# Kernel optimization log

Hardware: AMD Instinct MI355X
Metric: run time of the kernel (lower is better)

## Reference

```python
import jax, jax.numpy as jnp
import numpy as np

B, N_MAX = 32, 256          # graphs, max nodes per graph (uniform here)
L, D, H, Q, P, F = 4, 256, 8, 4, 16, 32  # layers, hidden, heads, q_dim, pe_dim, phi hidden
NEG = -1e9


def _dense_pos(batch, num_graphs):
    # position of each node inside its (sorted) graph segment
    counts = jax.ops.segment_sum(jnp.ones_like(batch), batch, num_segments=num_graphs)
    starts = jnp.concatenate([jnp.zeros((1,), batch.dtype), jnp.cumsum(counts)[:-1]])
    return jnp.arange(batch.shape[0]) - starts[batch]


def setup_inputs() -> dict:
    key = jax.random.key(0)
    ks = jax.random.split(key, 24)
    N = B * N_MAX
    E = N * 16
    s = 1.0 / np.sqrt(D)
    inp = {
        "x": jax.random.normal(ks[0], (N, D), jnp.float32),
        "z": jax.random.normal(ks[1], (N, Q, P, 2), jnp.float32) * 0.1,
        "Lambda": jax.random.uniform(ks[2], (B, Q, P), jnp.float32),
        "edge_attr": jax.random.normal(ks[3], (E, 16), jnp.float32),
        # attention projections per layer
        "Wq": jax.random.normal(ks[4], (L, D, D), jnp.float32) * s,
        "Wk": jax.random.normal(ks[5], (L, D, D), jnp.float32) * s,
        "Wv": jax.random.normal(ks[6], (L, D, D), jnp.float32) * s,
        "Wo": jax.random.normal(ks[7], (L, D, D), jnp.float32) * s,
        "bq": jnp.zeros((L, D), jnp.float32),
        "bk": jnp.zeros((L, D), jnp.float32),
        "bv": jnp.zeros((L, D), jnp.float32),
        "bo": jnp.zeros((L, D), jnp.float32),
        # eigenvalue MLP (DenseComplexNetwork, SPE-style) per layer
        "phi_W1": jax.random.normal(ks[8], (L, 1, F), jnp.float32),
        "phi_b1": jnp.zeros((L, F), jnp.float32),
        "phi_W2": jax.random.normal(ks[9], (L, F, H), jnp.float32) / np.sqrt(F),
        "phi_b2": jnp.zeros((L, H), jnp.float32),
        # BatchNorm1d affine params per layer
        "bn_gamma": jnp.ones((L, D), jnp.float32),
        "bn_beta": jnp.zeros((L, D), jnp.float32),
        # int inputs
        "edge_index": jax.random.randint(ks[10], (2, E), 0, N),
        "batch": jnp.repeat(jnp.arange(B), N_MAX),
    }
    return inp


def reference(x, z, Lambda, edge_attr, Wq, Wk, Wv, Wo, bq, bk, bv, bo,
              phi_W1, phi_b1, phi_W2, phi_b2, bn_gamma, bn_beta,
              edge_index, batch):
    # edge_index / edge_attr are unused by the original forward as well.
    dh = D // H
    pos = _dense_pos(batch, B)
    mask = jnp.zeros((B, N_MAX), bool).at[batch, pos].set(True)      # [B, n]
    zd = jnp.zeros((B, N_MAX, Q, P, 2), z.dtype).at[batch, pos].set(z)
    zr, zi = zd[..., 0], zd[..., 1]                                   # [B, n, Q, P]

    h0 = x
    for i in range(L):
        # ---- to_dense_batch ----
        hd = jnp.zeros((B, N_MAX, D), x.dtype).at[batch, pos].set(h0)
        # ---- DenseComplexNetwork: phi(Lambda), Re(V diag(phi) V^H) per head ----
        hphi = jax.nn.relu(Lambda[..., None] * phi_W1[i][0] + phi_b1[i])      # [B,Q,P,F]
        phi = jnp.einsum('bqpf,fh->bqph', hphi, phi_W2[i]) + phi_b2[i]        # [B,Q,P,H]
        bias = (jnp.einsum('bqph,biqp,bjqp->bhij', phi, zr, zr)
                + jnp.einsum('bqph,biqp,bjqp->bhij', phi, zi, zi))            # [B,H,n,n]
        # ---- multi-head attention with additive bias + key padding mask ----
        q = (hd @ Wq[i] + bq[i]).reshape(B, N_MAX, H, dh)
        k = (hd @ Wk[i] + bk[i]).reshape(B, N_MAX, H, dh)
        v = (hd @ Wv[i] + bv[i]).reshape(B, N_MAX, H, dh)
        scores = jnp.einsum('bihd,bjhd->bhij', q, k) / jnp.sqrt(jnp.float32(dh)) + bias
        scores = jnp.where(mask[:, None, None, :], scores, NEG)
        attn = jax.nn.softmax(scores, axis=-1)
        o = jnp.einsum('bhij,bjhd->bihd', attn, v).reshape(B, N_MAX, D) @ Wo[i] + bo[i]
        # ---- scatter back (h[mask]), residual, BatchNorm1d (batch stats) ----
        h = o[batch, pos] + h0                                                # [N, D]
        mean = h.mean(axis=0)
        var = ((h - mean) ** 2).mean(axis=0)
        h = (h - mean) / jnp.sqrt(var + 1e-5) * bn_gamma[i] + bn_beta[i]
        h0 = h
    return (h0, z)
```

## Files before the change

### kernel.cpp

```cpp
#include <hip/hip_runtime.h>
#include <hip/hip_bf16.h>

typedef __hip_bfloat16 bf16;
typedef __attribute__((ext_vector_type(8))) short short8v;
typedef __attribute__((ext_vector_type(4))) float f32x4;

constexpr int NB  = 32;
constexpr int NM  = 256;
constexpr int DD  = 256;
constexpr int NH  = 8;
constexpr int QP  = 64;
constexpr int FF  = 32;
constexpr int NT  = NB * NM;
constexpr int HD2 = NT * DD;
constexpr float QSCALE = 0.17677669529663687f;

__device__ __forceinline__ float b2f(unsigned short u) {
  return __uint_as_float(((unsigned)u) << 16);
}
__device__ __forceinline__ short f2b(float f) {
  union { bf16 h; short s; } u;
  u.h = __float2bfloat16(f);
  return u.s;
}

__global__ __launch_bounds__(256) void k_init(const float* __restrict__ z,
                                              float* __restrict__ outz,
                                              short* __restrict__ zbf,
                                              float* __restrict__ bna) {
  const int idx = blockIdx.x * 256 + threadIdx.x;
  const float4 v = ((const float4*)z)[idx];
  ((float4*)outz)[idx] = v;
  short4 s;
  s.x = f2b(v.x); s.y = f2b(v.y); s.z = f2b(v.z); s.w = f2b(v.w);
  ((short4*)zbf)[idx] = s;
  if (idx < 4 * 512) bna[idx] = 0.f;
}

__global__ __launch_bounds__(256) void k_wt(const float* __restrict__ Wq,
                                            const float* __restrict__ Wk,
                                            const float* __restrict__ Wv,
                                            const float* __restrict__ Wo,
                                            short* __restrict__ Wt) {
  __shared__ float Ts[32][33];
  const int mat = blockIdx.x;
  const int l = mat >> 2, wsel = mat & 3;
  const float* W = (wsel == 0 ? Wq : wsel == 1 ? Wk : wsel == 2 ? Wv : Wo) + l * DD * DD;
  const int j0 = blockIdx.y * 32;
  short* out = Wt + (size_t)mat * DD * DD;
  const int t = threadIdx.x;
  const int jj = t & 31, kk8 = t >> 5;
  for (int k0 = 0; k0 < DD; k0 += 32) {
    __syncthreads();
#pragma unroll
    for (int s = 0; s < 4; ++s) {
      const int kl = s * 8 + kk8;
      Ts[kl][jj] = W[(k0 + kl) * DD + j0 + jj];
    }
    __syncthreads();
#pragma unroll
    for (int s = 0; s < 4; ++s) {
      const int jl = (t >> 5) + s * 8;
      const int kl = t & 31;
      out[(size_t)(j0 + jl) * DD + k0 + kl] = f2b(Ts[kl][jl]);
    }
  }
}

__global__ __launch_bounds__(256) void k_phi_all(const float* __restrict__ Lam,
                                                 const float* __restrict__ W1,
                                                 const float* __restrict__ b1,
                                                 const float* __restrict__ W2,
                                                 const float* __restrict__ b2,
                                                 float* __restrict__ phiAll) {
  const int l = blockIdx.y;
  const int t = blockIdx.x * 256 + threadIdx.x;
  const int b = t >> 6, qp = t & 63;
  const float lam = Lam[b * QP + qp];
  const float* w1 = W1 + l * FF;
  const float* bb1 = b1 + l * FF;
  const float* w2 = W2 + l * FF * NH;
  const float* bb2 = b2 + l * NH;
  float acc[NH];
#pragma unroll
  for (int h = 0; h < NH; ++h) acc[h] = bb2[h];
  for (int f = 0; f < FF; ++f) {
    float a = lam * w1[f] + bb1[f];
    a = a > 0.f ? a : 0.f;
#pragma unroll
    for (int h = 0; h < NH; ++h) acc[h] += a * w2[f * NH + h];
  }
#pragma unroll
  for (int h = 0; h < NH; ++h)
    phiAll[(((size_t)l * NB + b) * NH + h) * QP + qp] = acc[h];
}

__global__ __launch_bounds__(256) void k_proj(const float* __restrict__ hsrc,
                                              const short* __restrict__ WtL,
                                              const float* __restrict__ bnstat,
                                              const float* __restrict__ gamma,
                                              const float* __restrict__ beta,
                                              const float* __restrict__ b0,
                                              const float* __restrict__ b1,
                                              const float* __restrict__ b2,
                                              short* __restrict__ o0,
                                              short* __restrict__ o1,
                                              short* __restrict__ o2) {
  __shared__ __align__(16) short As[128 * 128];
  __shared__ __align__(16) short Bs[128 * 128];
  __shared__ float bnsc[256], bnsh[256];
  const int t = threadIdx.x;
  const int m0 = blockIdx.x * 128;
  const int j0 = blockIdx.y * 128;
  const int zz = blockIdx.z;
  const short* W = WtL + (size_t)zz * DD * DD;
  const float* bb = zz == 0 ? b0 : zz == 1 ? b1 : b2;
  short* obf = zz == 0 ? o0 : zz == 1 ? o1 : o2;
  const float scale = (zz == 0) ? QSCALE : 1.0f;

  if (t < 256) {
    float sc = 1.f, sh = 0.f;
    if (bnstat) {
      const float mean = bnstat[t] * (1.0f / NT);
      const float var = bnstat[256 + t] * (1.0f / NT) - mean * mean;
      const float rstd = rsqrtf(var + 1e-5f);
      sc = rstd * gamma[t];
      sh = beta[t] - mean * sc;
    }
    bnsc[t] = sc; bnsh[t] = sh;
  }

  const int lane = t & 63, w = t >> 6;
  const int wr = w >> 1, wc = w & 1;
  const int fr = lane & 15, fq = lane >> 4;

  f32x4 acc[4][4] = {};

  for (int kb = 0; kb < 2; ++kb) {
    __syncthreads();
#pragma unroll
    for (int p = 0; p < 8; ++p) {
      const int c = p * 256 + t;
      const int r = c >> 4, ch = c & 15;
      const int sw = ((ch ^ (r & 7)) << 4);
      const int col0 = kb * 128 + ch * 8;
      const float* src = hsrc + (size_t)(m0 + r) * 256 + col0;
      const float4 v0 = *(const float4*)src;
      const float4 v1 = *(const float4*)(src + 4);
      short8v o;
      o[0] = f2b(v0.x * bnsc[col0 + 0] + bnsh[col0 + 0]);
      o[1] = f2b(v0.y * bnsc[col0 + 1] + bnsh[col0 + 1]);
      o[2] = f2b(v0.z * bnsc[col0 + 2] + bnsh[col0 + 2]);
      o[3] = f2b(v0.w * bnsc[col0 + 3] + bnsh[col0 + 3]);
      o[4] = f2b(v1.x * bnsc[col0 + 4] + bnsh[col0 + 4]);
      o[5] = f2b(v1.y * bnsc[col0 + 5] + bnsh[col0 + 5]);
      o[6] = f2b(v1.z * bnsc[col0 + 6] + bnsh[col0 + 6]);
      o[7] = f2b(v1.w * bnsc[col0 + 7] + bnsh[col0 + 7]);
      *(short8v*)((char*)As + r * 256 + sw) = o;
      *(short8v*)((char*)Bs + r * 256 + sw) =
          *(const short8v*)(W + (size_t)(j0 + r) * 256 + kb * 128 + ch * 8);
    }
    __syncthreads();
#pragma unroll
    for (int ks = 0; ks < 4; ++ks) {
      short8v a[4], bfrag[4];
#pragma unroll
      for (int m = 0; m < 4; ++m) {
        const int rA = wr * 64 + m * 16 + fr;
        a[m] = *(const short8v*)((const char*)As + rA * 256 + (((ks * 4 + fq) ^ (rA & 7)) << 4));
        const int rB = wc * 64 + m * 16 + fr;
        bfrag[m] = *(const short8v*)((const char*)Bs + rB * 256 + (((ks * 4 + fq) ^ (rB & 7)) << 4));
      }
#pragma unroll
      for (int m = 0; m < 4; ++m)
#pragma unroll
        for (int n = 0; n < 4; ++n)
          acc[m][n] = __builtin_amdgcn_mfma_f32_16x16x32_bf16(a[m], bfrag[n], acc[m][n], 0, 0, 0);
    }
  }
#pragma unroll
  for (int n = 0; n < 4; ++n) {
    const int col = j0 + wc * 64 + n * 16 + fr;
    const float bv = bb[col];
#pragma unroll
    for (int m = 0; m < 4; ++m) {
#pragma unroll
      for (int rr = 0; rr < 4; ++rr) {
        const int row = m0 + wr * 64 + m * 16 + fq * 4 + rr;
        obf[(size_t)row * 256 + col] = f2b((acc[m][n][rr] + bv) * scale);
      }
    }
  }
}

__global__ __launch_bounds__(256) void k_projo(const short* __restrict__ Abf,
                                               const short* __restrict__ WtO,
                                               const float* __restrict__ bo,
                                               const float* __restrict__ hin,
                                               float* __restrict__ hout,
                                               const float* __restrict__ bnstat,
                                               const float* __restrict__ gamma,
                                               const float* __restrict__ beta,
                                               float* __restrict__ bna) {
  __shared__ __align__(16) short As[64 * 128];
  __shared__ __align__(16) short Bs[128 * 128];
  __shared__ float sred[2][128][2];
  __shared__ float bnsc[256], bnsh[256];
  const int t = threadIdx.x;
  const int m0 = blockIdx.x * 64;
  const int c0 = blockIdx.y * 128;
  const int lane = t & 63, w = t >> 6;
  const int wr = w >> 1, wc = w & 1;
  const int fr = lane & 15, fq = lane >> 4;

  if (t < 256) {
    float sc = 1.f, sh = 0.f;
    if (bnstat) {
      const float mean = bnstat[t] * (1.0f / NT);
      const float var = bnstat[256 + t] * (1.0f / NT) - mean * mean;
      const float rstd = rsqrtf(var + 1e-5f);
      sc = rstd * gamma[t];
      sh = beta[t] - mean * sc;
    }
    bnsc[t] = sc; bnsh[t] = sh;
  }

  f32x4 acc[2][4] = {};
  for (int kb = 0; kb < 2; ++kb) {
    __syncthreads();
#pragma unroll
    for (int p = 0; p < 4; ++p) {
      const int c = p * 256 + t;
      const int r = c >> 4, ch = c & 15;
      const int sw = ((ch ^ (r & 7)) << 4);
      *(short8v*)((char*)As + r * 256 + sw) =
          *(const short8v*)(Abf + (size_t)(m0 + r) * 256 + kb * 128 + ch * 8);
    }
#pragma unroll
    for (int p = 0; p < 8; ++p) {
      const int c = p * 256 + t;
      const int r = c >> 4, ch = c & 15;
      const int sw = ((ch ^ (r & 7)) << 4);
      *(short8v*)((char*)Bs + r * 256 + sw) =
          *(const short8v*)(WtO + (size_t)(c0 + r) * 256 + kb * 128 + ch * 8);
    }
    __syncthreads();
#pragma unroll
    for (int ks = 0; ks < 4; ++ks) {
      short8v a[2], bfrag[4];
#pragma unroll
      for (int m = 0; m < 2; ++m) {
        const int rA = wr * 32 + m * 16 + fr;
        a[m] = *(const short8v*)((const char*)As + rA * 256 + (((ks * 4 + fq) ^ (rA & 7)) << 4));
      }
#pragma unroll
      for (int n = 0; n < 4; ++n) {
        const int rB = wc * 64 + n * 16 + fr;
        bfrag[n] = *(const short8v*)((const char*)Bs + rB * 256 + (((ks * 4 + fq) ^ (rB & 7)) << 4));
      }
#pragma unroll
      for (int m = 0; m < 2; ++m)
#pragma unroll
        for (int n = 0; n < 4; ++n)
          acc[m][n] = __builtin_amdgcn_mfma_f32_16x16x32_bf16(a[m], bfrag[n], acc[m][n], 0, 0, 0);
    }
  }
#pragma unroll
  for (int n = 0; n < 4; ++n) {
    const int col = c0 + wc * 64 + n * 16 + fr;
    const float bv = bo[col];
    const float sc = bnsc[col], sh = bnsh[col];
    float s = 0.f, ss = 0.f;
#pragma unroll
    for (int m = 0; m < 2; ++m) {
#pragma unroll
      for (int rr = 0; rr < 4; ++rr) {
        const int row = m0 + wr * 32 + m * 16 + fq * 4 + rr;
        const size_t idx = (size_t)row * 256 + col;
        const float v = acc[m][n][rr] + bv + (hin[idx] * sc + sh);
        hout[idx] = v;
        s += v;
        ss += v * v;
      }
    }
    s += __shfl_xor(s, 16); s += __shfl_xor(s, 32);
    ss += __shfl_xor(ss, 16); ss += __shfl_xor(ss, 32);
    if (fq == 0) {
      sred[wr][wc * 64 + n * 16 + fr][0] = s;
      sred[wr][wc * 64 + n * 16 + fr][1] = ss;
    }
  }
  __syncthreads();
  if (t < 128) {
    const float s = sred[0][t][0] + sred[1][t][0];
    const float ss = sred[0][t][1] + sred[1][t][1];
    atomicAdd(&bna[c0 + t], s);
    atomicAdd(&bna[256 + c0 + t], ss);
  }
}

__global__ __launch_bounds__(512, 2) void k_attn2(const short* __restrict__ qbf,
                                                  const short* __restrict__ kbf,
                                                  const short* __restrict__ vbf,
                                                  const short* __restrict__ zbf,
                                                  const float* __restrict__ phiAll,
                                                  short* __restrict__ obf, int l) {
  __shared__ __align__(16) char Ks[256 * 384];
  __shared__ __align__(16) char Vt[32 * 512];
  __shared__ __align__(16) char Pw[8 * 2 * 2560];
  __shared__ float rs_l[8 * 32];
  __shared__ float ph2[128];
  const int t = threadIdx.x;
  const int bh = blockIdx.x;
  const int b = bh >> 3, hh = bh & 7;
  const int bnode = b * 256;

  if (t < 128)
    ph2[t] = phiAll[(((size_t)l * NB + b) * NH + hh) * QP + (t >> 1)];
  __syncthreads();
  {
    const int r = t >> 1, half = t & 1;
    const size_t rowbase = (size_t)(bnode + r) * 256 + hh * 32;
#pragma unroll
    for (int j2 = 0; j2 < 2; ++j2) {
      const int c = half * 2 + j2;
      short8v v = *(const short8v*)(kbf + rowbase + c * 8);
      *(short8v*)(Ks + r * 384 + ((c ^ (r & 7)) << 4)) = v;
    }
    const short* zrow = zbf + (size_t)(bnode + r) * 128 + half * 64;
#pragma unroll
    for (int cc = 0; cc < 8; ++cc) {
      const short8v zv = *(const short8v*)(zrow + cc * 8);
      const int zc = half * 64 + cc * 8;
      short8v o;
#pragma unroll
      for (int e = 0; e < 8; ++e)
        o[e] = f2b(b2f((unsigned short)zv[e]) * ph2[zc + e]);
      const int c = 4 + half * 8 + cc;
      *(short8v*)(Ks + r * 384 + ((c ^ (r & 7)) << 4)) = o;
    }
    const short* vrow = vbf + rowbase + half * 16;
    short8v v0 = *(const short8v*)(vrow);
    short8v v1 = *(const short8v*)(vrow + 8);
#pragma unroll
    for (int dd = 0; dd < 16; ++dd) {
      const int d = half * 16 + dd;
      const short val = dd < 8 ? v0[dd] : v1[dd - 8];
      *(short*)(Vt + d * 512 + (((r >> 3) ^ (d & 7)) << 4) + (r & 7) * 2) = val;
    }
  }
  __syncthreads();

  const int lane = t & 63, w = t >> 6;
  const int fr = lane & 15, fq = lane >> 4;
  const int i0w = w * 32;

  short8v Qf[2][5];
#pragma unroll
  for (int s = 0; s < 2; ++s) {
    const int node = bnode + i0w + s * 16 + fr;
    Qf[s][0] = *(const short8v*)(qbf + (size_t)node * 256 + hh * 32 + fq * 8);
    const short* zr = zbf + (size_t)node * 128;
#pragma unroll
    for (int ks = 1; ks < 5; ++ks)
      Qf[s][ks] = *(const short8v*)(zr + (ks - 1) * 32 + fq * 8);
  }

  f32x4 acc[2][16] = {};
#pragma unroll
  for (int ks = 0; ks < 5; ++ks) {
#pragma unroll
    for (int jt = 0; jt < 16; ++jt) {
      const int row = jt * 16 + fr;
      const short8v a = *(const short8v*)(Ks + row * 384 + (((ks * 4 + fq) ^ (row & 7)) << 4));
      acc[0][jt] = __builtin_amdgcn_mfma_f32_16x16x32_bf16(a, Qf[0][ks], acc[0][jt], 0, 0, 0);
      acc[1][jt] = __builtin_amdgcn_mfma_f32_16x16x32_bf16(a, Qf[1][ks], acc[1][jt], 0, 0, 0);
    }
  }

  float rsv0, rsv1;
#pragma unroll
  for (int s = 0; s < 2; ++s) {
    float m = -1e30f;
#pragma unroll
    for (int jt = 0; jt < 16; ++jt)
#pragma unroll
      for (int rr = 0; rr < 4; ++rr) m = fmaxf(m, acc[s][jt][rr]);
    m = fmaxf(m, __shfl_xor(m, 16));
    m = fmaxf(m, __shfl_xor(m, 32));
    float sm = 0.f;
#pragma unroll
    for (int jt = 0; jt < 16; ++jt)
#pragma unroll
      for (int rr = 0; rr < 4; ++rr) {
        const float e = __expf(acc[s][jt][rr] - m);
        acc[s][jt][rr] = e;
        sm += e;
      }
    sm += __shfl_xor(sm, 16);
    sm += __shfl_xor(sm, 32);
    const float r = 1.0f / sm;
    if (s == 0) rsv0 = r; else rsv1 = r;
  }
  if (fq == 0) rs_l[w * 32 + fr] = rsv0;
  if (fq == 1) rs_l[w * 32 + 16 + fr] = rsv1;

  f32x4 oac[2][2] = {};
  char* pw0 = Pw + w * 5120;
#pragma unroll
  for (int ks = 0; ks < 8; ++ks) {
    char* pw = pw0 + (ks & 1) * 2560;
#pragma unroll
    for (int s = 0; s < 2; ++s) {
#pragma unroll
      for (int j2 = 0; j2 < 2; ++j2) {
        const int jt = ks * 2 + j2;
        short4 pk;
        pk.x = f2b(acc[s][jt][0]); pk.y = f2b(acc[s][jt][1]);
        pk.z = f2b(acc[s][jt][2]); pk.w = f2b(acc[s][jt][3]);
        *(short4*)(pw + (s * 16 + fr) * 80 + j2 * 32 + fq * 8) = pk;
      }
    }
    asm volatile("s_waitcnt lgkmcnt(0)" ::: "memory");
    __builtin_amdgcn_sched_barrier(0);
    const short8v pa0 = *(const short8v*)(pw + fr * 80 + fq * 16);
    const short8v pa1 = *(const short8v*)(pw + (16 + fr) * 80 + fq * 16);
    const int sw = (((ks * 4 + fq) ^ (fr & 7)) << 4);
    const short8v vb0 = *(const short8v*)(Vt + fr * 512 + sw);
    const short8v vb1 = *(const short8v*)(Vt + (16 + fr) * 512 + sw);
    oac[0][0] = __builtin_amdgcn_mfma_f32_16x16x32_bf16(pa0, vb0, oac[0][0], 0, 0, 0);
    oac[0][1] = __builtin_amdgcn_mfma_f32_16x16x32_bf16(pa0, vb1, oac[0][1], 0, 0, 0);
    oac[1][0] = __builtin_amdgcn_mfma_f32_16x16x32_bf16(pa1, vb0, oac[1][0], 0, 0, 0);
    oac[1][1] = __builtin_amdgcn_mfma_f32_16x16x32_bf16(pa1, vb1, oac[1][1], 0, 0, 0);
  }

#pragma unroll
  for (int s = 0; s < 2; ++s) {
#pragma unroll
    for (int rr = 0; rr < 4; ++rr) {
      const float rs = rs_l[w * 32 + s * 16 + fq * 4 + rr];
      const int node = bnode + i0w + s * 16 + fq * 4 + rr;
#pragma unroll
      for (int nt = 0; nt < 2; ++nt)
        obf[(size_t)node * 256 + hh * 32 + nt * 16 + fr] = f2b(oac[s][nt][rr] * rs);
    }
  }
}

__global__ __launch_bounds__(256) void k_bn_apply(const float* __restrict__ h,
                                                  const float* __restrict__ accum,
                                                  const float* __restrict__ gamma,
                                                  const float* __restrict__ beta,
                                                  float* __restrict__ outp, int l) {
  const int idx = blockIdx.x * 256 + threadIdx.x;
  const int col = idx & 255;
  const float mean = accum[col] * (1.0f / NT);
  const float var = accum[DD + col] * (1.0f / NT) - mean * mean;
  const float rstd = rsqrtf(var + 1e-5f);
  outp[idx] = (h[idx] - mean) * rstd * gamma[l * DD + col] + beta[l * DD + col];
}

extern "C" void kernel_launch(void* const* d_in, const int* in_sizes, int n_in,
                              void* d_out, int out_size, void* d_ws, size_t ws_size,
                              hipStream_t stream) {
  (void)in_sizes; (void)n_in; (void)out_size; (void)ws_size;
  const float* x    = (const float*)d_in[0];
  const float* z    = (const float*)d_in[1];
  const float* Lam  = (const float*)d_in[2];
  const float* Wq   = (const float*)d_in[4];
  const float* Wk   = (const float*)d_in[5];
  const float* Wv   = (const float*)d_in[6];
  const float* Wo   = (const float*)d_in[7];
  const float* bq   = (const float*)d_in[8];
  const float* bk   = (const float*)d_in[9];
  const float* bv   = (const float*)d_in[10];
  const float* bo   = (const float*)d_in[11];
  const float* pW1  = (const float*)d_in[12];
  const float* pb1  = (const float*)d_in[13];
  const float* pW2  = (const float*)d_in[14];
  const float* pb2  = (const float*)d_in[15];
  const float* gam  = (const float*)d_in[16];
  const float* bet  = (const float*)d_in[17];
  float* out = (float*)d_out;

  float* h    = (float*)d_ws;
  short* qbf  = (short*)(h + HD2);
  short* kbf  = qbf + HD2;
  short* vbf  = kbf + HD2;
  short* obf  = vbf + HD2;
  short* zbf  = obf + HD2;
  short* Wt   = zbf + NT * 128;
  float* phiA = (float*)(Wt + 16 * DD * DD);
  float* bna  = phiA + 4 * NB * NH * QP;

  k_init<<<1024, 256, 0, stream>>>(z, out + HD2, zbf, bna);
  k_wt<<<dim3(16, 8), 256, 0, stream>>>(Wq, Wk, Wv, Wo, Wt);
  k_phi_all<<<dim3(8, 4), 256, 0, stream>>>(Lam, pW1, pb1, pW2, pb2, phiA);
  for (int l = 0; l < 4; ++l) {
    const float* bnprev = l ? bna + (l - 1) * 512 : nullptr;
    const float* gprev  = l ? gam + (l - 1) * DD : gam;
    const float* bprev  = l ? bet + (l - 1) * DD : bet;
    const float* hsrc   = l ? h : x;
    k_proj<<<dim3(64, 2, 3), 256, 0, stream>>>(hsrc, Wt + (size_t)l * 4 * DD * DD,
                                               bnprev, gprev, bprev,
                                               bq + l * DD, bk + l * DD, bv + l * DD,
                                               qbf, kbf, vbf);
    k_attn2<<<256, 512, 0, stream>>>(qbf, kbf, vbf, zbf, phiA, obf, l);
    k_projo<<<dim3(128, 2), 256, 0, stream>>>(obf, Wt + (size_t)(l * 4 + 3) * DD * DD,
                                              bo + l * DD, hsrc, h,
                                              bnprev, gprev, bprev, bna + l * 512);
  }
  k_bn_apply<<<8192, 256, 0, stream>>>(h, bna + 3 * 512, gam, bet, out, 3);
}
```

Before: 169.4 us.

## Fuse setup kernels and share BN-converted activation tile across QKV projections

Merges the three setup kernels (z copy and bf16 convert, weight transpose, phi MLP) into one launch to cut launch overhead. Replaces the QKV projection kernel, which re-read and re-normalized the fp32 activations once per matrix, with one that loads a 64-row, full-K activation tile once into LDS and loops over Q, K and V weights. This cuts global activation reads and BN/convert work by about a factor of three, but each block now runs three serial GEMMs with smaller M tiles, giving fewer MFMAs per weight load. The grid drops from 384 to 256 blocks.

```diff
diff --git a/kernel.cpp b/kernel.cpp
--- a/kernel.cpp
+++ b/kernel.cpp
@@ -24,100 +24,9 @@
   return u.s;
 }
 
-__global__ __launch_bounds__(256) void k_init(const float* __restrict__ z,
-                                              float* __restrict__ outz,
-                                              short* __restrict__ zbf,
-                                              float* __restrict__ bna) {
-  const int idx = blockIdx.x * 256 + threadIdx.x;
-  const float4 v = ((const float4*)z)[idx];
-  ((float4*)outz)[idx] = v;
-  short4 s;
-  s.x = f2b(v.x); s.y = f2b(v.y); s.z = f2b(v.z); s.w = f2b(v.w);
-  ((short4*)zbf)[idx] = s;
-  if (idx < 4 * 512) bna[idx] = 0.f;
-}
-
-__global__ __launch_bounds__(256) void k_wt(const float* __restrict__ Wq,
-                                            const float* __restrict__ Wk,
-                                            const float* __restrict__ Wv,
-                                            const float* __restrict__ Wo,
-                                            short* __restrict__ Wt) {
-  __shared__ float Ts[32][33];
-  const int mat = blockIdx.x;
-  const int l = mat >> 2, wsel = mat & 3;
-  const float* W = (wsel == 0 ? Wq : wsel == 1 ? Wk : wsel == 2 ? Wv : Wo) + l * DD * DD;
-  const int j0 = blockIdx.y * 32;
-  short* out = Wt + (size_t)mat * DD * DD;
-  const int t = threadIdx.x;
-  const int jj = t & 31, kk8 = t >> 5;
-  for (int k0 = 0; k0 < DD; k0 += 32) {
-    __syncthreads();
-#pragma unroll
-    for (int s = 0; s < 4; ++s) {
-      const int kl = s * 8 + kk8;
-      Ts[kl][jj] = W[(k0 + kl) * DD + j0 + jj];
-    }
-    __syncthreads();
-#pragma unroll
-    for (int s = 0; s < 4; ++s) {
-      const int jl = (t >> 5) + s * 8;
-      const int kl = t & 31;
-      out[(size_t)(j0 + jl) * DD + k0 + kl] = f2b(Ts[kl][jl]);
-    }
-  }
-}
-
-__global__ __launch_bounds__(256) void k_phi_all(const float* __restrict__ Lam,
-                                                 const float* __restrict__ W1,
-                                                 const float* __restrict__ b1,
-                                                 const float* __restrict__ W2,
-                                                 const float* __restrict__ b2,
-                                                 float* __restrict__ phiAll) {
-  const int l = blockIdx.y;
-  const int t = blockIdx.x * 256 + threadIdx.x;
-  const int b = t >> 6, qp = t & 63;
-  const float lam = Lam[b * QP + qp];
-  const float* w1 = W1 + l * FF;
-  const float* bb1 = b1 + l * FF;
-  const float* w2 = W2 + l * FF * NH;
-  const float* bb2 = b2 + l * NH;
-  float acc[NH];
-#pragma unroll
-  for (int h = 0; h < NH; ++h) acc[h] = bb2[h];
-  for (int f = 0; f < FF; ++f) {
-    float a = lam * w1[f] + bb1[f];
-    a = a > 0.f ? a : 0.f;
-#pragma unroll
-    for (int h = 0; h < NH; ++h) acc[h] += a * w2[f * NH + h];
-  }
-#pragma unroll
-  for (int h = 0; h < NH; ++h)
-    phiAll[(((size_t)l * NB + b) * NH + h) * QP + qp] = acc[h];
-}
-
-__global__ __launch_bounds__(256) void k_proj(const float* __restrict__ hsrc,
-                                              const short* __restrict__ WtL,
-                                              const float* __restrict__ bnstat,
-                                              const float* __restrict__ gamma,
-                                              const float* __restrict__ beta,
-                                              const float* __restrict__ b0,
-                                              const float* __restrict__ b1,
-                                              const float* __restrict__ b2,
-                                              short* __restrict__ o0,
-                                              short* __restrict__ o1,
-                                              short* __restrict__ o2) {
-  __shared__ __align__(16) short As[128 * 128];
-  __shared__ __align__(16) short Bs[128 * 128];
-  __shared__ float bnsc[256], bnsh[256];
-  const int t = threadIdx.x;
-  const int m0 = blockIdx.x * 128;
-  const int j0 = blockIdx.y * 128;
-  const int zz = blockIdx.z;
-  const short* W = WtL + (size_t)zz * DD * DD;
-  const float* bb = zz == 0 ? b0 : zz == 1 ? b1 : b2;
-  short* obf = zz == 0 ? o0 : zz == 1 ? o1 : o2;
-  const float scale = (zz == 0) ? QSCALE : 1.0f;
-
+__device__ __forceinline__ void bn_coeffs(const float* bnstat, const float* gamma,
+                                          const float* beta, float* bnsc, float* bnsh,
+                                          int t) {
   if (t < 256) {
     float sc = 1.f, sh = 0.f;
     if (bnstat) {
@@ -129,66 +38,173 @@
     }
     bnsc[t] = sc; bnsh[t] = sh;
   }
+}
+
+__global__ __launch_bounds__(256) void k_setup(const float* __restrict__ z,
+                                               float* __restrict__ outz,
+                                               short* __restrict__ zbf,
+                                               float* __restrict__ bna,
+                                               const float* __restrict__ Lam,
+                                               const float* __restrict__ pW1,
+                                               const float* __restrict__ pb1,
+                                               const float* __restrict__ pW2,
+                                               const float* __restrict__ pb2,
+                                               float* __restrict__ phiA,
+                                               const float* __restrict__ Wq,
+                                               const float* __restrict__ Wk,
+                                               const float* __restrict__ Wv,
+                                               const float* __restrict__ Wo,
+                                               short* __restrict__ Wt) {
+  __shared__ float Ts[32][33];
+  const int t = threadIdx.x;
+  const int idx = blockIdx.x * 256 + t;
+  {
+    const float4 v = ((const float4*)z)[idx];
+    ((float4*)outz)[idx] = v;
+    short4 s;
+    s.x = f2b(v.x); s.y = f2b(v.y); s.z = f2b(v.z); s.w = f2b(v.w);
+    ((short4*)zbf)[idx] = s;
+  }
+  if (idx < 4 * 512) bna[idx] = 0.f;
+  if (idx < 4 * 2048) {
+    const int l = idx >> 11;
+    const int t2 = idx & 2047;
+    const int b = t2 >> 6, qp = t2 & 63;
+    const float lam = Lam[b * QP + qp];
+    const float* w1 = pW1 + l * FF;
+    const float* bb1 = pb1 + l * FF;
+    const float* w2 = pW2 + l * FF * NH;
+    const float* bb2 = pb2 + l * NH;
+    float acc[NH];
+#pragma unroll
+    for (int h = 0; h < NH; ++h) acc[h] = bb2[h];
+    for (int f = 0; f < FF; ++f) {
+      float a = lam * w1[f] + bb1[f];
+      a = a > 0.f ? a : 0.f;
+#pragma unroll
+      for (int h = 0; h < NH; ++h) acc[h] += a * w2[f * NH + h];
+    }
+#pragma unroll
+    for (int h = 0; h < NH; ++h)
+      phiA[(((size_t)l * NB + b) * NH + h) * QP + qp] = acc[h];
+  }
+  if (blockIdx.x < 128) {
+    const int mat = blockIdx.x >> 3;
+    const int l = mat >> 2, wsel = mat & 3;
+    const float* W = (wsel == 0 ? Wq : wsel == 1 ? Wk : wsel == 2 ? Wv : Wo) + l * DD * DD;
+    const int j0 = (blockIdx.x & 7) * 32;
+    short* outw = Wt + (size_t)mat * DD * DD;
+    const int jj = t & 31, kk8 = t >> 5;
+    for (int k0 = 0; k0 < DD; k0 += 32) {
+      __syncthreads();
+#pragma unroll
+      for (int s = 0; s < 4; ++s) {
+        const int kl = s * 8 + kk8;
+        Ts[kl][jj] = W[(k0 + kl) * DD + j0 + jj];
+      }
+      __syncthreads();
+#pragma unroll
+      for (int s = 0; s < 4; ++s) {
+        const int jl = (t >> 5) + s * 8;
+        const int kl = t & 31;
+        outw[(size_t)(j0 + jl) * DD + k0 + kl] = f2b(Ts[kl][jl]);
+      }
+    }
+  }
+}
+
+__global__ __launch_bounds__(256) void k_proj3(const float* __restrict__ hsrc,
+                                               const short* __restrict__ WtL,
+                                               const float* __restrict__ bnstat,
+                                               const float* __restrict__ gamma,
+                                               const float* __restrict__ beta,
+                                               const float* __restrict__ bq,
+                                               const float* __restrict__ bk,
+                                               const float* __restrict__ bv,
+                                               short* __restrict__ qbf,
+                                               short* __restrict__ kbf,
+                                               short* __restrict__ vbf) {
+  __shared__ __align__(16) char As[64 * 512];
+  __shared__ __align__(16) char Bs[128 * 256];
+  __shared__ float bnsc[256], bnsh[256];
+  const int t = threadIdx.x;
+  const int m0 = blockIdx.x * 64;
+  const int j0 = blockIdx.y * 128;
+  bn_coeffs(bnstat, gamma, beta, bnsc, bnsh, t);
+  __syncthreads();
+
+#pragma unroll
+  for (int p = 0; p < 8; ++p) {
+    const int c = p * 256 + t;
+    const int r = c >> 5, ch = c & 31;
+    const int col0 = ch * 8;
+    const float* src = hsrc + (size_t)(m0 + r) * 256 + col0;
+    const float4 v0 = *(const float4*)src;
+    const float4 v1 = *(const float4*)(src + 4);
+    short8v o;
+    o[0] = f2b(v0.x * bnsc[col0 + 0] + bnsh[col0 + 0]);
+    o[1] = f2b(v0.y * bnsc[col0 + 1] + bnsh[col0 + 1]);
+    o[2] = f2b(v0.z * bnsc[col0 + 2] + bnsh[col0 + 2]);
+    o[3] = f2b(v0.w * bnsc[col0 + 3] + bnsh[col0 + 3]);
+    o[4] = f2b(v1.x * bnsc[col0 + 4] + bnsh[col0 + 4]);
+    o[5] = f2b(v1.y * bnsc[col0 + 5] + bnsh[col0 + 5]);
+    o[6] = f2b(v1.z * bnsc[col0 + 6] + bnsh[col0 + 6]);
+    o[7] = f2b(v1.w * bnsc[col0 + 7] + bnsh[col0 + 7]);
+    *(short8v*)(As + r * 512 + ((ch ^ (r & 7)) << 4)) = o;
+  }
 
   const int lane = t & 63, w = t >> 6;
   const int wr = w >> 1, wc = w & 1;
   const int fr = lane & 15, fq = lane >> 4;
 
-  f32x4 acc[4][4] = {};
-
-  for (int kb = 0; kb < 2; ++kb) {
-    __syncthreads();
-#pragma unroll
-    for (int p = 0; p < 8; ++p) {
-      const int c = p * 256 + t;
-      const int r = c >> 4, ch = c & 15;
-      const int sw = ((ch ^ (r & 7)) << 4);
-      const int col0 = kb * 128 + ch * 8;
-      const float* src = hsrc + (size_t)(m0 + r) * 256 + col0;
-      const float4 v0 = *(const float4*)src;
-      const float4 v1 = *(const float4*)(src + 4);
-      short8v o;
-      o[0] = f2b(v0.x * bnsc[col0 + 0] + bnsh[col0 + 0]);
-      o[1] = f2b(v0.y * bnsc[col0 + 1] + bnsh[col0 + 1]);
-      o[2] = f2b(v0.z * bnsc[col0 + 2] + bnsh[col0 + 2]);
-      o[3] = f2b(v0.w * bnsc[col0 + 3] + bnsh[col0 + 3]);
-      o[4] = f2b(v1.x * bnsc[col0 + 4] + bnsh[col0 + 4]);
-      o[5] = f2b(v1.y * bnsc[col0 + 5] + bnsh[col0 + 5]);
-      o[6] = f2b(v1.z * bnsc[col0 + 6] + bnsh[col0 + 6]);
-      o[7] = f2b(v1.w * bnsc[col0 + 7] + bnsh[col0 + 7]);
-      *(short8v*)((char*)As + r * 256 + sw) = o;
-      *(short8v*)((char*)Bs + r * 256 + sw) =
-          *(const short8v*)(W + (size_t)(j0 + r) * 256 + kb * 128 + ch * 8);
-    }
-    __syncthreads();
-#pragma unroll
-    for (int ks = 0; ks < 4; ++ks) {
-      short8v a[4], bfrag[4];
-#pragma unroll
-      for (int m = 0; m < 4; ++m) {
-        const int rA = wr * 64 + m * 16 + fr;
-        a[m] = *(const short8v*)((const char*)As + rA * 256 + (((ks * 4 + fq) ^ (rA & 7)) << 4));
-        const int rB = wc * 64 + m * 16 + fr;
-        bfrag[m] = *(const short8v*)((const char*)Bs + rB * 256 + (((ks * 4 + fq) ^ (rB & 7)) << 4));
-      }
-#pragma unroll
-      for (int m = 0; m < 4; ++m)
-#pragma unroll
-        for (int n = 0; n < 4; ++n)
-          acc[m][n] = __builtin_amdgcn_mfma_f32_16x16x32_bf16(a[m], bfrag[n], acc[m][n], 0, 0, 0);
-    }
-  }
-#pragma unroll
-  for (int n = 0; n < 4; ++n) {
-    const int col = j0 + wc * 64 + n * 16 + fr;
-    const float bv = bb[col];
-#pragma unroll
-    for (int m = 0; m < 4; ++m) {
-#pragma unroll
-      for (int rr = 0; rr < 4; ++rr) {
-        const int row = m0 + wr * 64 + m * 16 + fq * 4 + rr;
-        obf[(size_t)row * 256 + col] = f2b((acc[m][n][rr] + bv) * scale);
-      }
+  for (int mat = 0; mat < 3; ++mat) {
+    const short* W = WtL + (size_t)mat * DD * DD;
+    const float* bb = mat == 0 ? bq : mat == 1 ? bk : bv;
+    short* obf = mat == 0 ? qbf : mat == 1 ? kbf : vbf;
+    const float scale = mat == 0 ? QSCALE : 1.0f;
+    f32x4 acc[2][4] = {};
+    for (int kb = 0; kb < 2; ++kb) {
+      __syncthreads();
+#pragma unroll
+      for (int p = 0; p < 8; ++p) {
+        const int c = p * 256 + t;
+        const int r = c >> 4, ch = c & 15;
+        *(short8v*)(Bs + r * 256 + ((ch ^ (r & 7)) << 4)) =
+            *(const short8v*)(W + (size_t)(j0 + r) * 256 + kb * 128 + ch * 8);
+      }
+      __syncthreads();
+#pragma unroll
+      for (int ks = 0; ks < 4; ++ks) {
+        short8v a[2], bfrag[4];
+#pragma unroll
+        for (int m = 0; m < 2; ++m) {
+          const int rA = wr * 32 + m * 16 + fr;
+          const int chA = kb * 16 + ks * 4 + fq;
+          a[m] = *(const short8v*)(As + rA * 512 + ((chA ^ (rA & 7)) << 4));
+        }
+#pragma unroll
+        for (int n = 0; n < 4; ++n) {
+          const int rB = wc * 64 + n * 16 + fr;
+          bfrag[n] = *(const short8v*)(Bs + rB * 256 + (((ks * 4 + fq) ^ (rB & 7)) << 4));
+        }
+#pragma unroll
+        for (int m = 0; m < 2; ++m)
+#pragma unroll
+          for (int n = 0; n < 4; ++n)
+            acc[m][n] = __builtin_amdgcn_mfma_f32_16x16x32_bf16(a[m], bfrag[n], acc[m][n], 0, 0, 0);
+      }
+    }
+#pragma unroll
+    for (int n = 0; n < 4; ++n) {
+      const int col = j0 + wc * 64 + n * 16 + fr;
+      const float bv2 = bb[col];
+#pragma unroll
+      for (int m = 0; m < 2; ++m)
+#pragma unroll
+        for (int rr = 0; rr < 4; ++rr) {
+          const int row = m0 + wr * 32 + m * 16 + fq * 4 + rr;
+          obf[(size_t)row * 256 + col] = f2b((acc[m][n][rr] + bv2) * scale);
+        }
     }
   }
 }
@@ -213,17 +229,7 @@
   const int wr = w >> 1, wc = w & 1;
   const int fr = lane & 15, fq = lane >> 4;
 
-  if (t < 256) {
-    float sc = 1.f, sh = 0.f;
-    if (bnstat) {
-      const float mean = bnstat[t] * (1.0f / NT);
-      const float var = bnstat[256 + t] * (1.0f / NT) - mean * mean;
-      const float rstd = rsqrtf(var + 1e-5f);
-      sc = rstd * gamma[t];
-      sh = beta[t] - mean * sc;
-    }
-    bnsc[t] = sc; bnsh[t] = sh;
-  }
+  bn_coeffs(bnstat, gamma, beta, bnsc, bnsh, t);
 
   f32x4 acc[2][4] = {};
   for (int kb = 0; kb < 2; ++kb) {
@@ -272,7 +278,7 @@
     const float sc = bnsc[col], sh = bnsh[col];
     float s = 0.f, ss = 0.f;
 #pragma unroll
-    for (int m = 0; m < 2; ++m) {
+    for (int m = 0; m < 2; ++m)
 #pragma unroll
       for (int rr = 0; rr < 4; ++rr) {
         const int row = m0 + wr * 32 + m * 16 + fq * 4 + rr;
@@ -282,7 +288,6 @@
         s += v;
         ss += v * v;
       }
-    }
     s += __shfl_xor(s, 16); s += __shfl_xor(s, 32);
     ss += __shfl_xor(ss, 16); ss += __shfl_xor(ss, 32);
     if (fq == 0) {
@@ -411,7 +416,7 @@
   for (int ks = 0; ks < 8; ++ks) {
     char* pw = pw0 + (ks & 1) * 2560;
 #pragma unroll
-    for (int s = 0; s < 2; ++s) {
+    for (int s = 0; s < 2; ++s)
 #pragma unroll
       for (int j2 = 0; j2 < 2; ++j2) {
         const int jt = ks * 2 + j2;
@@ -420,7 +425,6 @@
         pk.z = f2b(acc[s][jt][2]); pk.w = f2b(acc[s][jt][3]);
         *(short4*)(pw + (s * 16 + fr) * 80 + j2 * 32 + fq * 8) = pk;
       }
-    }
     asm volatile("s_waitcnt lgkmcnt(0)" ::: "memory");
     __builtin_amdgcn_sched_barrier(0);
     const short8v pa0 = *(const short8v*)(pw + fr * 80 + fq * 16);
@@ -435,7 +439,7 @@
   }
 
 #pragma unroll
-  for (int s = 0; s < 2; ++s) {
+  for (int s = 0; s < 2; ++s)
 #pragma unroll
     for (int rr = 0; rr < 4; ++rr) {
       const float rs = rs_l[w * 32 + s * 16 + fq * 4 + rr];
@@ -444,7 +448,6 @@
       for (int nt = 0; nt < 2; ++nt)
         obf[(size_t)node * 256 + hh * 32 + nt * 16 + fr] = f2b(oac[s][nt][rr] * rs);
     }
-  }
 }
 
 __global__ __launch_bounds__(256) void k_bn_apply(const float* __restrict__ h,
@@ -493,18 +496,17 @@
   float* phiA = (float*)(Wt + 16 * DD * DD);
   float* bna  = phiA + 4 * NB * NH * QP;
 
-  k_init<<<1024, 256, 0, stream>>>(z, out + HD2, zbf, bna);
-  k_wt<<<dim3(16, 8), 256, 0, stream>>>(Wq, Wk, Wv, Wo, Wt);
-  k_phi_all<<<dim3(8, 4), 256, 0, stream>>>(Lam, pW1, pb1, pW2, pb2, phiA);
+  k_setup<<<1024, 256, 0, stream>>>(z, out + HD2, zbf, bna, Lam, pW1, pb1, pW2, pb2,
+                                    phiA, Wq, Wk, Wv, Wo, Wt);
   for (int l = 0; l < 4; ++l) {
     const float* bnprev = l ? bna + (l - 1) * 512 : nullptr;
-    const float* gprev  = l ? gam + (l - 1) * DD : gam;
-    const float* bprev  = l ? bet + (l - 1) * DD : bet;
+    const float* gprev  = gam + (l ? (l - 1) * DD : 0);
+    const float* bprev  = bet + (l ? (l - 1) * DD : 0);
     const float* hsrc   = l ? h : x;
-    k_proj<<<dim3(64, 2, 3), 256, 0, stream>>>(hsrc, Wt + (size_t)l * 4 * DD * DD,
-                                               bnprev, gprev, bprev,
-                                               bq + l * DD, bk + l * DD, bv + l * DD,
-                                               qbf, kbf, vbf);
+    k_proj3<<<dim3(128, 2), 256, 0, stream>>>(hsrc, Wt + (size_t)l * 4 * DD * DD,
+                                              bnprev, gprev, bprev,
+                                              bq + l * DD, bk + l * DD, bv + l * DD,
+                                              qbf, kbf, vbf);
     k_attn2<<<256, 512, 0, stream>>>(qbf, kbf, vbf, zbf, phiA, obf, l);
     k_projo<<<dim3(128, 2), 256, 0, stream>>>(obf, Wt + (size_t)(l * 4 + 3) * DD * DD,
                                               bo + l * DD, hsrc, h,
```

Measured after the change: 176.1 us. 4.0% more time.
